# Optimization experiments

Hardware: AMD Instinct MI355X
Metric: run time of the kernel (lower is better)

The kernel has to match this reference:

```python
import jax, jax.numpy as jnp
import numpy as np

COMMITMENT_COST = 0.25
CODEBOOK_SIZE = 1024
EMBED_DIM = 128


def setup_inputs() -> dict:
    key = jax.random.key(0)
    k1, k2 = jax.random.split(key)
    z = jax.random.normal(k1, (16, 2048, EMBED_DIM), dtype=jnp.float32)
    codebook = jax.random.normal(k2, (CODEBOOK_SIZE, EMBED_DIM), dtype=jnp.float32) / (EMBED_DIM ** 0.5)
    return {"z": z, "codebook": codebook}


def reference(z, codebook):
    B, N, D = z.shape
    K = codebook.shape[0]
    flat = z.reshape(-1, D)  # [M, D]

    distances = (
        jnp.sum(flat * flat, axis=1, keepdims=True)
        - 2.0 * flat @ codebook.T
        + jnp.sum(codebook * codebook, axis=1)[None, :]
    )
    indices = jnp.argmin(distances, axis=1)  # [M]

    # one_hot @ codebook == direct gather
    quantized = codebook[indices].reshape(B, N, D)

    codebook_loss = jnp.mean((quantized - z) ** 2)
    commit_loss = COMMITMENT_COST * jnp.mean((z - quantized) ** 2)

    # straight-through (no grad in pure fwd, same values)
    z_q = quantized

    # avg_probs = mean of one-hot encodings = code usage frequency
    M = flat.shape[0]
    counts = jax.ops.segment_sum(jnp.ones((M,), dtype=z.dtype), indices, num_segments=K)
    avg_probs = counts / M
    perplexity = jnp.exp(-jnp.sum(avg_probs * jnp.log(avg_probs + 1e-10)))

    return (
        z_q,
        indices.reshape(B, N),
        commit_loss,
        codebook_loss,
        perplexity,
        distances.reshape(B, N, K),
    )
```

## Files before the change

kernel.cpp:

```cpp
#include <hip/hip_runtime.h>
#include <math.h>

#define D 128
#define K 1024
#define BM 32
#define BN 32
#define NCH (K / BN)
#define CHB 16384

typedef __attribute__((ext_vector_type(8))) short bf16x8;
typedef __attribute__((ext_vector_type(4))) float f32x4;
typedef unsigned short u16;


__device__ __forceinline__ u16 f2bf(float x) {
    union { float f; unsigned u; } v; v.f = x;
    unsigned r = (v.u + 0x7FFFu + ((v.u >> 16) & 1u)) >> 16;
    return (u16)r;
}
__device__ __forceinline__ float bf2f(u16 b) {
    union { float f; unsigned u; } v; v.u = ((unsigned)b) << 16;
    return v.f;
}
__device__ __forceinline__ void gll16(const void* g, void* l) {
    __builtin_amdgcn_global_load_lds(
        (const __attribute__((address_space(1))) void*)g,
        (__attribute__((address_space(3))) void*)l, 16, 0, 0);
}

__global__ void prep_cb(const float* __restrict__ cb, u16* __restrict__ frag,
                        float* __restrict__ cnorm) {
    int tid = blockIdx.x * blockDim.x + threadIdx.x;
    int code = tid >> 5, d4 = tid & 31;
    float4 v = reinterpret_cast<const float4*>(cb)[tid];
    u16 h0 = f2bf(v.x), h1 = f2bf(v.y), h2 = f2bf(v.z), h3 = f2bf(v.w);
    u16 l0 = f2bf(v.x - bf2f(h0)), l1 = f2bf(v.y - bf2f(h1));
    u16 l2 = f2bf(v.z - bf2f(h2)), l3 = f2bf(v.w - bf2f(h3));
    int c = code >> 5, row = code & 31;
    int sb = (row * 256 + d4 * 8) ^ ((row & 7) << 4);
    char* base = (char*)frag + (size_t)c * CHB;
    *reinterpret_cast<ushort4*>(base + sb) = make_ushort4(h0, h1, h2, h3);
    *reinterpret_cast<ushort4*>(base + 8192 + sb) = make_ushort4(l0, l1, l2, l3);
    float s = v.x * v.x + v.y * v.y + v.z * v.z + v.w * v.w;
#pragma unroll
    for (int m = 1; m <= 16; m <<= 1) s += __shfl_xor(s, m);
    if (d4 == 0) cnorm[code] = s;
}

__global__ __launch_bounds__(256, 4)
void vq_main(const float* __restrict__ z, const float* __restrict__ codebook,
             const float* __restrict__ cnorm, const u16* __restrict__ frag,
             int* __restrict__ hist, float* __restrict__ loss_accum,
             float* __restrict__ out_zq, float* __restrict__ out_idx,
             float* __restrict__ out_dist) {
    __shared__ u16 Bsh[2][8192];
    __shared__ float cn_s[K];
    __shared__ float xn_s[BM];
    __shared__ int bi_s[BM], si_s[BM], best_s[BM];

    const int t = threadIdx.x;
    const int lane = t & 63;
    const int wave = t >> 6;
    const int lr = lane & 15, lg = lane >> 4;
    const int rowgrp = wave & 1, colhalf = wave >> 1;
    const int row_base = blockIdx.x * BM;

    if (t < BM) xn_s[t] = 0.f;
#pragma unroll
    for (int k = 0; k < 4; ++k) cn_s[t + k * 256] = cnorm[t + k * 256];
    __syncthreads();

    {
        const float4* zg = reinterpret_cast<const float4*>(z + (size_t)row_base * D);
#pragma unroll
        for (int k = 0; k < 4; ++k) {
            int f = t + k * 256;
            int r = f >> 5, d4 = f & 31;
            float4 v = zg[f];
            u16 h0 = f2bf(v.x), h1 = f2bf(v.y), h2 = f2bf(v.z), h3 = f2bf(v.w);
            u16 l0 = f2bf(v.x - bf2f(h0)), l1 = f2bf(v.y - bf2f(h1));
            u16 l2 = f2bf(v.z - bf2f(h2)), l3 = f2bf(v.w - bf2f(h3));
            int sb = (r * 256 + d4 * 8) ^ ((r & 7) << 4);
            *reinterpret_cast<ushort4*>((char*)Bsh + sb) = make_ushort4(h0, h1, h2, h3);
            *reinterpret_cast<ushort4*>((char*)Bsh + 8192 + sb) = make_ushort4(l0, l1, l2, l3);
            atomicAdd(&xn_s[r], v.x * v.x + v.y * v.y + v.z * v.z + v.w * v.w);
        }
    }
    __syncthreads();

    const int arow = rowgrp * 16 + lr;
    bf16x8 zh[4], zl[4];
#pragma unroll
    for (int kb = 0; kb < 4; ++kb) {
        int sb = (arow * 256 + kb * 64 + lg * 16) ^ ((arow & 7) << 4);
        zh[kb] = *reinterpret_cast<const bf16x8*>((char*)Bsh + sb);
        zl[kb] = *reinterpret_cast<const bf16x8*>((char*)Bsh + 8192 + sb);
    }
    const float xn = xn_s[arow];

    const char* fsrc = (const char*)frag + t * 16;
    {
        char* dst = (char*)Bsh + 16384 + t * 16;
#pragma unroll
        for (int it = 0; it < 4; ++it) gll16(fsrc + it * 4096, dst + it * 4096);
    }
    __syncthreads();

    float v1 = INFINITY, v2 = INFINITY;
    int i1 = K, i2 = K;
    int cur = 1;
    const int myrow = row_base + rowgrp * 16 + lr;
    float* orow = out_dist + (size_t)myrow * K + colhalf * 16 + lg * 4;
    const int crow = colhalf * 16 + lr;

    for (int c = 0; c < NCH; ++c) {
        if (c < NCH - 1) {
            const char* src = fsrc + (size_t)(c + 1) * CHB;
            char* dst = (char*)Bsh + (cur ^ 1) * 16384 + t * 16;
#pragma unroll
            for (int it = 0; it < 4; ++it) gll16(src + it * 4096, dst + it * 4096);
        }

        const char* bb = (const char*)Bsh + cur * 16384;
        f32x4 acc = {0.f, 0.f, 0.f, 0.f};
#pragma unroll
        for (int kb = 0; kb < 4; ++kb) {
            int sb = (crow * 256 + kb * 64 + lg * 16) ^ ((crow & 7) << 4);
            bf16x8 ch = *reinterpret_cast<const bf16x8*>(bb + sb);
            bf16x8 cl = *reinterpret_cast<const bf16x8*>(bb + 8192 + sb);
            acc = __builtin_amdgcn_mfma_f32_16x16x32_bf16(ch, zh[kb], acc, 0, 0, 0);
            acc = __builtin_amdgcn_mfma_f32_16x16x32_bf16(ch, zl[kb], acc, 0, 0, 0);
            acc = __builtin_amdgcn_mfma_f32_16x16x32_bf16(cl, zh[kb], acc, 0, 0, 0);
        }

        const int cbase = c * BN + colhalf * 16 + lg * 4;
        float4 cn4 = *reinterpret_cast<const float4*>(&cn_s[cbase]);
        float d0 = fmaf(-2.f, acc[0], xn + cn4.x);
        float d1 = fmaf(-2.f, acc[1], xn + cn4.y);
        float d2 = fmaf(-2.f, acc[2], xn + cn4.z);
        float d3 = fmaf(-2.f, acc[3], xn + cn4.w);
        if (d0 < v1) { v2 = v1; i2 = i1; v1 = d0; i1 = cbase; }
        else if (d0 < v2) { v2 = d0; i2 = cbase; }
        if (d1 < v1) { v2 = v1; i2 = i1; v1 = d1; i1 = cbase + 1; }
        else if (d1 < v2) { v2 = d1; i2 = cbase + 1; }
        if (d2 < v1) { v2 = v1; i2 = i1; v1 = d2; i1 = cbase + 2; }
        else if (d2 < v2) { v2 = d2; i2 = cbase + 2; }
        if (d3 < v1) { v2 = v1; i2 = i1; v1 = d3; i1 = cbase + 3; }
        else if (d3 < v2) { v2 = d3; i2 = cbase + 3; }
        *reinterpret_cast<float4*>(orow + (size_t)c * BN) = make_float4(d0, d1, d2, d3);

        __syncthreads();
        cur ^= 1;
    }

    float* rv1 = reinterpret_cast<float*>(Bsh);
    float* rv2 = rv1 + 256;
    int* ri1 = reinterpret_cast<int*>(rv2 + 256);
    int* ri2 = ri1 + 256;
    {
        const int slot = colhalf * 4 + lg;
        const int rr = rowgrp * 16 + lr;
        rv1[slot * 32 + rr] = v1;
        rv2[slot * 32 + rr] = v2;
        ri1[slot * 32 + rr] = i1;
        ri2[slot * 32 + rr] = i2;
    }
    __syncthreads();

    if (t < BM) {
        float bv = INFINITY, sv = INFINITY;
        int bi = K, si = K;
        for (int s = 0; s < 8; ++s) {
            float cv1 = rv1[s * 32 + t]; int ci1 = ri1[s * 32 + t];
            float cv2 = rv2[s * 32 + t]; int ci2 = ri2[s * 32 + t];
            if (cv1 < bv || (cv1 == bv && ci1 < bi)) { sv = bv; si = bi; bv = cv1; bi = ci1; }
            else if (cv1 < sv || (cv1 == sv && ci1 < si)) { sv = cv1; si = ci1; }
            if (cv2 < bv || (cv2 == bv && ci2 < bi)) { sv = bv; si = bi; bv = cv2; bi = ci2; }
            else if (cv2 < sv || (cv2 == sv && ci2 < si)) { sv = cv2; si = ci2; }
        }
        bi_s[t] = bi;
        si_s[t] = si;
    }
    __syncthreads();

    float lossv = 0.f;
    if (t < 128) {
        const int rr = t >> 2, t4 = t & 3;
        const int bi = bi_s[rr], si = si_s[rr];
        const float4* zr = reinterpret_cast<const float4*>(z + (size_t)(row_base + rr) * D);
        const float4* c1 = reinterpret_cast<const float4*>(codebook + (size_t)bi * D);
        const float4* c2 = reinterpret_cast<const float4*>(codebook + (size_t)si * D);
        double dd1 = 0.0, dd2 = 0.0;
#pragma unroll
        for (int j = 0; j < 8; ++j) {
            float4 xv = zr[t4 * 8 + j];
            float4 a = c1[t4 * 8 + j];
            float4 b = c2[t4 * 8 + j];
            double e;
            e = (double)xv.x - (double)a.x; dd1 += e * e;
            e = (double)xv.y - (double)a.y; dd1 += e * e;
            e = (double)xv.z - (double)a.z; dd1 += e * e;
            e = (double)xv.w - (double)a.w; dd1 += e * e;
            e = (double)xv.x - (double)b.x; dd2 += e * e;
            e = (double)xv.y - (double)b.y; dd2 += e * e;
            e = (double)xv.z - (double)b.z; dd2 += e * e;
            e = (double)xv.w - (double)b.w; dd2 += e * e;
        }
        dd1 += __shfl_xor(dd1, 1); dd1 += __shfl_xor(dd1, 2);
        dd2 += __shfl_xor(dd2, 1); dd2 += __shfl_xor(dd2, 2);
        if (t4 == 0) {
            int fi = bi; double dmin = dd1;
            if (dd2 < dd1 || (dd2 == dd1 && si < bi)) { fi = si; dmin = dd2; }
            best_s[rr] = fi;
            out_idx[row_base + rr] = (float)fi;
            atomicAdd(&hist[fi], 1);
            lossv = (float)dmin;
        }
    }
#pragma unroll
    for (int o = 32; o > 0; o >>= 1) lossv += __shfl_down(lossv, o);
    if (lane == 0) atomicAdd(loss_accum, lossv);
    __syncthreads();

    {
        const float4* cb4 = reinterpret_cast<const float4*>(codebook);
        float4* zq4 = reinterpret_cast<float4*>(out_zq + (size_t)row_base * D);
#pragma unroll
        for (int k = 0; k < 4; ++k) {
            int f = t + k * 256;
            int r = f >> 5, d4 = f & 31;
            zq4[f] = cb4[(size_t)best_s[r] * 32 + d4];
        }
    }
}

__global__ void vq_finalize(const int* __restrict__ hist, const float* __restrict__ loss_accum,
                            float* __restrict__ out_scalars, int M) {
    __shared__ float red[256];
    int t = threadIdx.x;
    float s = 0.f;
    float invM = 1.0f / (float)M;
#pragma unroll
    for (int k = 0; k < K / 256; ++k) {
        float p = (float)hist[t + k * 256] * invM;
        s += p * logf(p + 1e-10f);
    }
    red[t] = s;
    __syncthreads();
    for (int off = 128; off > 0; off >>= 1) {
        if (t < off) red[t] += red[t + off];
        __syncthreads();
    }
    if (t == 0) {
        float loss = loss_accum[0] / ((float)M * (float)D);
        out_scalars[0] = 0.25f * loss;
        out_scalars[1] = loss;
        out_scalars[2] = expf(-red[0]);
    }
}

extern "C" void kernel_launch(void* const* d_in, const int* in_sizes, int n_in,
                              void* d_out, int out_size, void* d_ws, size_t ws_size,
                              hipStream_t stream) {
    const float* z = (const float*)d_in[0];
    const float* codebook = (const float*)d_in[1];
    int M = in_sizes[0] / D;

    float* out = (float*)d_out;
    float* out_zq = out;
    float* out_idx = out + (size_t)M * D;
    float* out_scalars = out_idx + M;
    float* out_dist = out_scalars + 3;

    int* hist = (int*)d_ws;
    float* loss_accum = (float*)((char*)d_ws + 4096);
    float* cnorm = (float*)((char*)d_ws + 8192);
    u16* frag = (u16*)((char*)d_ws + 16384);

    hipMemsetAsync(d_ws, 0, 8192, stream);
    prep_cb<<<(K * D / 4) / 256, 256, 0, stream>>>(codebook, frag, cnorm);
    vq_main<<<M / BM, 256, 0, stream>>>(z, codebook, cnorm, frag, hist, loss_accum,
                                        out_zq, out_idx, out_dist);
    vq_finalize<<<1, 256, 0, stream>>>(hist, loss_accum, out_scalars, M);
}
```

Before: 114.4 us.

## Hold codebook fragments in registers and split distance and merge kernels

```diff
diff --git a/kernel.cpp b/kernel.cpp
--- a/kernel.cpp
+++ b/kernel.cpp
@@ -3,30 +3,265 @@
 
 #define D 128
 #define K 1024
+
+typedef __attribute__((ext_vector_type(8))) short bf16x8;
+typedef __attribute__((ext_vector_type(4))) float f32x4;
+typedef unsigned short u16;
+
+
+__device__ __forceinline__ u16 f2bf(float x) {
+    union { float f; unsigned u; } v; v.f = x;
+    unsigned r = (v.u + 0x7FFFu + ((v.u >> 16) & 1u)) >> 16;
+    return (u16)r;
+}
+__device__ __forceinline__ float bf2f(u16 b) {
+    union { float f; unsigned u; } v; v.u = ((unsigned)b) << 16;
+    return v.f;
+}
+__device__ __forceinline__ void gll16(const void* g, void* l) {
+    __builtin_amdgcn_global_load_lds(
+        (const __attribute__((address_space(1))) void*)g,
+        (__attribute__((address_space(3))) void*)l, 16, 0, 0);
+}
+
+__device__ __forceinline__ void t2merge(float& v1, int& i1, float& v2, int& i2,
+                                        float bv1, int bi1, float bv2, int bi2) {
+    if (bv1 < v1 || (bv1 == v1 && bi1 < i1)) {
+        v2 = v1; i2 = i1;
+        v1 = bv1; i1 = bi1;
+        if (bv2 < v2 || (bv2 == v2 && bi2 < i2)) { v2 = bv2; i2 = bi2; }
+    } else {
+        if (bv1 < v2 || (bv1 == v2 && bi1 < i2)) { v2 = bv1; i2 = bi1; }
+    }
+}
+
+
+__global__ void prep2(const float* __restrict__ cb, u16* __restrict__ frag,
+                      float* __restrict__ cnorm) {
+    int tid = blockIdx.x * blockDim.x + threadIdx.x;
+    int code = tid >> 5, d4 = tid & 31;
+    float4 v = reinterpret_cast<const float4*>(cb)[tid];
+    u16 h0 = f2bf(v.x), h1 = f2bf(v.y), h2 = f2bf(v.z), h3 = f2bf(v.w);
+    u16 l0 = f2bf(v.x - bf2f(h0)), l1 = f2bf(v.y - bf2f(h1));
+    u16 l2 = f2bf(v.z - bf2f(h2)), l3 = f2bf(v.w - bf2f(h3));
+    u16* base = frag + (size_t)code * 256;
+    *reinterpret_cast<ushort4*>(base + d4 * 4) = make_ushort4(h0, h1, h2, h3);
+    *reinterpret_cast<ushort4*>(base + 128 + d4 * 4) = make_ushort4(l0, l1, l2, l3);
+    float s = v.x * v.x + v.y * v.y + v.z * v.z + v.w * v.w;
+#pragma unroll
+    for (int m = 1; m <= 16; m <<= 1) s += __shfl_xor(s, m);
+    if (d4 == 0) cnorm[code] = s;
+}
+
+__global__ __launch_bounds__(512, 8)
+void vq_dist(const float* __restrict__ z, const u16* __restrict__ frag,
+             const float* __restrict__ cnorm, float4* __restrict__ part,
+             float* __restrict__ out_dist) {
+    __shared__ u16 zsh[16384];
+    __shared__ float cn_s[512];
+    __shared__ float xn_s[64];
+
+    const int t = threadIdx.x;
+    const int lane = t & 63;
+    const int wave = t >> 6;
+    const int lr = lane & 15, lg = lane >> 4;
+    const int rg = blockIdx.x >> 1, cg = blockIdx.x & 1;
+    const int row_base = rg * 64;
+
+    if (t < 64) xn_s[t] = 0.f;
+    if (t < 512) cn_s[t] = cnorm[cg * 512 + t];
+    __syncthreads();
+
+    {
+        const float4* zg = reinterpret_cast<const float4*>(z + (size_t)row_base * D);
+#pragma unroll
+        for (int k = 0; k < 4; ++k) {
+            int f = t + k * 512;
+            int r = f >> 5, d4 = f & 31;
+            float4 v = zg[f];
+            u16 h0 = f2bf(v.x), h1 = f2bf(v.y), h2 = f2bf(v.z), h3 = f2bf(v.w);
+            u16 l0 = f2bf(v.x - bf2f(h0)), l1 = f2bf(v.y - bf2f(h1));
+            u16 l2 = f2bf(v.z - bf2f(h2)), l3 = f2bf(v.w - bf2f(h3));
+            int sb = (r * 256 + d4 * 8) ^ ((r & 7) << 4);
+            *reinterpret_cast<ushort4*>((char*)zsh + sb) = make_ushort4(h0, h1, h2, h3);
+            *reinterpret_cast<ushort4*>((char*)zsh + 16384 + sb) = make_ushort4(l0, l1, l2, l3);
+            atomicAdd(&xn_s[r], v.x * v.x + v.y * v.y + v.z * v.z + v.w * v.w);
+        }
+    }
+
+    bf16x8 ch[4][4], cl[4][4];
+    {
+        const u16* cbase = frag + (size_t)(cg * 512 + wave * 64) * 256;
+#pragma unroll
+        for (int nt = 0; nt < 4; ++nt)
+#pragma unroll
+            for (int kb = 0; kb < 4; ++kb) {
+                const u16* p = cbase + (size_t)(nt * 16 + lr) * 256 + kb * 32 + lg * 8;
+                ch[nt][kb] = *reinterpret_cast<const bf16x8*>(p);
+                cl[nt][kb] = *reinterpret_cast<const bf16x8*>(p + 128);
+            }
+    }
+    __syncthreads();
+
+    float v1[4], v2[4];
+    int i1[4], i2[4];
+#pragma unroll
+    for (int s = 0; s < 4; ++s) { v1[s] = INFINITY; v2[s] = INFINITY; i1[s] = K; i2[s] = K; }
+
+    const int code0 = cg * 512 + wave * 64;
+
+#pragma unroll
+    for (int s = 0; s < 4; ++s) {
+        f32x4 acc[4];
+#pragma unroll
+        for (int nt = 0; nt < 4; ++nt) { acc[nt][0] = 0.f; acc[nt][1] = 0.f; acc[nt][2] = 0.f; acc[nt][3] = 0.f; }
+
+#pragma unroll
+        for (int kb = 0; kb < 4; ++kb) {
+            int zrow = s * 16 + lr;
+            int sb = (zrow * 256 + kb * 64 + lg * 16) ^ ((zrow & 7) << 4);
+            bf16x8 zh = *reinterpret_cast<const bf16x8*>((char*)zsh + sb);
+            bf16x8 zl = *reinterpret_cast<const bf16x8*>((char*)zsh + 16384 + sb);
+#pragma unroll
+            for (int nt = 0; nt < 4; ++nt) {
+                acc[nt] = __builtin_amdgcn_mfma_f32_16x16x32_bf16(ch[nt][kb], zh, acc[nt], 0, 0, 0);
+                acc[nt] = __builtin_amdgcn_mfma_f32_16x16x32_bf16(ch[nt][kb], zl, acc[nt], 0, 0, 0);
+                acc[nt] = __builtin_amdgcn_mfma_f32_16x16x32_bf16(cl[nt][kb], zh, acc[nt], 0, 0, 0);
+            }
+        }
+
+        const int myrow = row_base + s * 16 + lr;
+        const float xn = xn_s[s * 16 + lr];
+        float* orow = out_dist + (size_t)myrow * K + code0 + lg * 4;
+#pragma unroll
+        for (int nt = 0; nt < 4; ++nt) {
+            float4 cn4 = *reinterpret_cast<const float4*>(&cn_s[wave * 64 + nt * 16 + lg * 4]);
+            int cb0 = code0 + nt * 16 + lg * 4;
+            float d0 = fmaf(-2.f, acc[nt][0], xn + cn4.x);
+            float d1 = fmaf(-2.f, acc[nt][1], xn + cn4.y);
+            float d2 = fmaf(-2.f, acc[nt][2], xn + cn4.z);
+            float d3 = fmaf(-2.f, acc[nt][3], xn + cn4.w);
+            if (d0 < v1[s]) { v2[s] = v1[s]; i2[s] = i1[s]; v1[s] = d0; i1[s] = cb0; }
+            else if (d0 < v2[s]) { v2[s] = d0; i2[s] = cb0; }
+            if (d1 < v1[s]) { v2[s] = v1[s]; i2[s] = i1[s]; v1[s] = d1; i1[s] = cb0 + 1; }
+            else if (d1 < v2[s]) { v2[s] = d1; i2[s] = cb0 + 1; }
+            if (d2 < v1[s]) { v2[s] = v1[s]; i2[s] = i1[s]; v1[s] = d2; i1[s] = cb0 + 2; }
+            else if (d2 < v2[s]) { v2[s] = d2; i2[s] = cb0 + 2; }
+            if (d3 < v1[s]) { v2[s] = v1[s]; i2[s] = i1[s]; v1[s] = d3; i1[s] = cb0 + 3; }
+            else if (d3 < v2[s]) { v2[s] = d3; i2[s] = cb0 + 3; }
+            f32x4 dv = {d0, d1, d2, d3};
+            __builtin_nontemporal_store(dv, reinterpret_cast<f32x4*>(orow + nt * 16));
+        }
+    }
+
+#pragma unroll
+    for (int s = 0; s < 4; ++s) {
+#pragma unroll
+        for (int m = 16; m <= 32; m <<= 1) {
+            float bv1 = __shfl_xor(v1[s], m), bv2 = __shfl_xor(v2[s], m);
+            int bi1 = __shfl_xor(i1[s], m), bi2 = __shfl_xor(i2[s], m);
+            t2merge(v1[s], i1[s], v2[s], i2[s], bv1, bi1, bv2, bi2);
+        }
+    }
+
+    __syncthreads();
+    float4* scr = reinterpret_cast<float4*>(zsh);
+    if (lane < 16) {
+#pragma unroll
+        for (int s = 0; s < 4; ++s) {
+            int row = s * 16 + lane;
+            float4 p;
+            p.x = v1[s]; p.y = v2[s];
+            p.z = __int_as_float(i1[s]); p.w = __int_as_float(i2[s]);
+            scr[row * 8 + wave] = p;
+        }
+    }
+    __syncthreads();
+
+    if (t < 64) {
+        float bv = INFINITY, sv = INFINITY;
+        int bi = K, si = K;
+        for (int w = 0; w < 8; ++w) {
+            float4 p = scr[t * 8 + w];
+            t2merge(bv, bi, sv, si, p.x, __float_as_int(p.z), p.y, __float_as_int(p.w));
+        }
+        float4 o;
+        o.x = bv; o.y = sv;
+        o.z = __int_as_float(bi); o.w = __int_as_float(si);
+        part[(size_t)(row_base + t) * 2 + cg] = o;
+    }
+}
+
+__global__ __launch_bounds__(256)
+void vq_merge(const float* __restrict__ z, const float* __restrict__ codebook,
+              const float4* __restrict__ part, int* __restrict__ hist,
+              float* __restrict__ loss_accum, float* __restrict__ out_zq,
+              float* __restrict__ out_idx) {
+    __shared__ int best_s[64];
+    const int t = threadIdx.x;
+    const int lane = t & 63;
+    const int row0 = blockIdx.x * 64;
+    const int rr = t >> 2, t4 = t & 3;
+    const int row = row0 + rr;
+
+    float4 pa = part[(size_t)row * 2];
+    float4 pb = part[(size_t)row * 2 + 1];
+    float v1 = pa.x, v2 = pa.y;
+    int i1 = __float_as_int(pa.z), i2 = __float_as_int(pa.w);
+    t2merge(v1, i1, v2, i2, pb.x, __float_as_int(pb.z), pb.y, __float_as_int(pb.w));
+    const int bi = i1, si = i2;
+
+    const float4* zr = reinterpret_cast<const float4*>(z + (size_t)row * D);
+    const float4* c1 = reinterpret_cast<const float4*>(codebook + (size_t)bi * D);
+    const float4* c2 = reinterpret_cast<const float4*>(codebook + (size_t)si * D);
+    double dd1 = 0.0, dd2 = 0.0;
+#pragma unroll
+    for (int j = 0; j < 8; ++j) {
+        float4 xv = zr[t4 * 8 + j];
+        float4 a = c1[t4 * 8 + j];
+        float4 b = c2[t4 * 8 + j];
+        double e;
+        e = (double)xv.x - (double)a.x; dd1 += e * e;
+        e = (double)xv.y - (double)a.y; dd1 += e * e;
+        e = (double)xv.z - (double)a.z; dd1 += e * e;
+        e = (double)xv.w - (double)a.w; dd1 += e * e;
+        e = (double)xv.x - (double)b.x; dd2 += e * e;
+        e = (double)xv.y - (double)b.y; dd2 += e * e;
+        e = (double)xv.z - (double)b.z; dd2 += e * e;
+        e = (double)xv.w - (double)b.w; dd2 += e * e;
+    }
+    dd1 += __shfl_xor(dd1, 1); dd1 += __shfl_xor(dd1, 2);
+    dd2 += __shfl_xor(dd2, 1); dd2 += __shfl_xor(dd2, 2);
+    float lossv = 0.f;
+    if (t4 == 0) {
+        int fi = bi; double dmin = dd1;
+        if (dd2 < dd1 || (dd2 == dd1 && si < bi)) { fi = si; dmin = dd2; }
+        best_s[rr] = fi;
+        out_idx[row] = (float)fi;
+        atomicAdd(&hist[fi], 1);
+        lossv = (float)dmin;
+    }
+#pragma unroll
+    for (int o = 32; o > 0; o >>= 1) lossv += __shfl_down(lossv, o);
+    if (lane == 0) atomicAdd(loss_accum, lossv);
+    __syncthreads();
+
+    const float4* cb4 = reinterpret_cast<const float4*>(codebook);
+    float4* zq4 = reinterpret_cast<float4*>(out_zq + (size_t)row0 * D);
+#pragma unroll
+    for (int k = 0; k < 8; ++k) {
+        int f = t + k * 256;
+        int r = f >> 5, d4 = f & 31;
+        float4 q = cb4[(size_t)best_s[r] * 32 + d4];
+        f32x4 qv = {q.x, q.y, q.z, q.w};
+        __builtin_nontemporal_store(qv, reinterpret_cast<f32x4*>(&zq4[f]));
+    }
+}
+
 #define BM 32
 #define BN 32
 #define NCH (K / BN)
 #define CHB 16384
-
-typedef __attribute__((ext_vector_type(8))) short bf16x8;
-typedef __attribute__((ext_vector_type(4))) float f32x4;
-typedef unsigned short u16;
-
-
-__device__ __forceinline__ u16 f2bf(float x) {
-    union { float f; unsigned u; } v; v.f = x;
-    unsigned r = (v.u + 0x7FFFu + ((v.u >> 16) & 1u)) >> 16;
-    return (u16)r;
-}
-__device__ __forceinline__ float bf2f(u16 b) {
-    union { float f; unsigned u; } v; v.u = ((unsigned)b) << 16;
-    return v.f;
-}
-__device__ __forceinline__ void gll16(const void* g, void* l) {
-    __builtin_amdgcn_global_load_lds(
-        (const __attribute__((address_space(1))) void*)g,
-        (__attribute__((address_space(3))) void*)l, 16, 0, 0);
-}
 
 __global__ void prep_cb(const float* __restrict__ cb, u16* __restrict__ frag,
                         float* __restrict__ cnorm) {
@@ -126,11 +361,11 @@
 #pragma unroll
         for (int kb = 0; kb < 4; ++kb) {
             int sb = (crow * 256 + kb * 64 + lg * 16) ^ ((crow & 7) << 4);
-            bf16x8 ch = *reinterpret_cast<const bf16x8*>(bb + sb);
-            bf16x8 cl = *reinterpret_cast<const bf16x8*>(bb + 8192 + sb);
-            acc = __builtin_amdgcn_mfma_f32_16x16x32_bf16(ch, zh[kb], acc, 0, 0, 0);
-            acc = __builtin_amdgcn_mfma_f32_16x16x32_bf16(ch, zl[kb], acc, 0, 0, 0);
-            acc = __builtin_amdgcn_mfma_f32_16x16x32_bf16(cl, zh[kb], acc, 0, 0, 0);
+            bf16x8 chh = *reinterpret_cast<const bf16x8*>(bb + sb);
+            bf16x8 cll = *reinterpret_cast<const bf16x8*>(bb + 8192 + sb);
+            acc = __builtin_amdgcn_mfma_f32_16x16x32_bf16(chh, zh[kb], acc, 0, 0, 0);
+            acc = __builtin_amdgcn_mfma_f32_16x16x32_bf16(chh, zl[kb], acc, 0, 0, 0);
+            acc = __builtin_amdgcn_mfma_f32_16x16x32_bf16(cll, zh[kb], acc, 0, 0, 0);
         }
 
         const int cbase = c * BN + colhalf * 16 + lg * 4;
@@ -171,12 +406,7 @@
         float bv = INFINITY, sv = INFINITY;
         int bi = K, si = K;
         for (int s = 0; s < 8; ++s) {
-            float cv1 = rv1[s * 32 + t]; int ci1 = ri1[s * 32 + t];
-            float cv2 = rv2[s * 32 + t]; int ci2 = ri2[s * 32 + t];
-            if (cv1 < bv || (cv1 == bv && ci1 < bi)) { sv = bv; si = bi; bv = cv1; bi = ci1; }
-            else if (cv1 < sv || (cv1 == sv && ci1 < si)) { sv = cv1; si = ci1; }
-            if (cv2 < bv || (cv2 == bv && ci2 < bi)) { sv = bv; si = bi; bv = cv2; bi = ci2; }
-            else if (cv2 < sv || (cv2 == sv && ci2 < si)) { sv = cv2; si = ci2; }
+            t2merge(bv, bi, sv, si, rv1[s * 32 + t], ri1[s * 32 + t], rv2[s * 32 + t], ri2[s * 32 + t]);
         }
         bi_s[t] = bi;
         si_s[t] = si;
@@ -276,10 +506,18 @@
     float* loss_accum = (float*)((char*)d_ws + 4096);
     float* cnorm = (float*)((char*)d_ws + 8192);
     u16* frag = (u16*)((char*)d_ws + 16384);
+    float4* part = (float4*)((char*)d_ws + 540672);
 
     hipMemsetAsync(d_ws, 0, 8192, stream);
-    prep_cb<<<(K * D / 4) / 256, 256, 0, stream>>>(codebook, frag, cnorm);
-    vq_main<<<M / BM, 256, 0, stream>>>(z, codebook, cnorm, frag, hist, loss_accum,
-                                        out_zq, out_idx, out_dist);
+    if (ws_size >= (size_t)540672 + (size_t)M * 32) {
+        prep2<<<(K * D / 4) / 256, 256, 0, stream>>>(codebook, frag, cnorm);
+        vq_dist<<<(M / 64) * 2, 512, 0, stream>>>(z, frag, cnorm, part, out_dist);
+        vq_merge<<<M / 64, 256, 0, stream>>>(z, codebook, part, hist, loss_accum,
+                                             out_zq, out_idx);
+    } else {
+        prep_cb<<<(K * D / 4) / 256, 256, 0, stream>>>(codebook, frag, cnorm);
+        vq_main<<<M / BM, 256, 0, stream>>>(z, codebook, cnorm, frag, hist, loss_accum,
+                                            out_zq, out_idx, out_dist);
+    }
     vq_finalize<<<1, 256, 0, stream>>>(hist, loss_accum, out_scalars, M);
 }
```

After: 445.6 us. 290% more time.

## Keep codebook fragments in registers and stream z rows from LDS

Applied to the files above, without the earlier changes.

```diff
diff --git a/kernel.cpp b/kernel.cpp
--- a/kernel.cpp
+++ b/kernel.cpp
@@ -3,10 +3,6 @@
 
 #define D 128
 #define K 1024
-#define BM 32
-#define BN 32
-#define NCH (K / BN)
-#define CHB 16384
 
 typedef __attribute__((ext_vector_type(8))) short bf16x8;
 typedef __attribute__((ext_vector_type(4))) float f32x4;
@@ -22,161 +18,162 @@
     union { float f; unsigned u; } v; v.u = ((unsigned)b) << 16;
     return v.f;
 }
-__device__ __forceinline__ void gll16(const void* g, void* l) {
-    __builtin_amdgcn_global_load_lds(
-        (const __attribute__((address_space(1))) void*)g,
-        (__attribute__((address_space(3))) void*)l, 16, 0, 0);
-}
-
-__global__ void prep_cb(const float* __restrict__ cb, u16* __restrict__ frag,
-                        float* __restrict__ cnorm) {
+
+__device__ __forceinline__ void t2merge(float& v1, int& i1, float& v2, int& i2,
+                                        float bv1, int bi1, float bv2, int bi2) {
+    if (bv1 < v1 || (bv1 == v1 && bi1 < i1)) {
+        v2 = v1; i2 = i1;
+        v1 = bv1; i1 = bi1;
+        if (bv2 < v2 || (bv2 == v2 && bi2 < i2)) { v2 = bv2; i2 = bi2; }
+    } else {
+        if (bv1 < v2 || (bv1 == v2 && bi1 < i2)) { v2 = bv1; i2 = bi1; }
+    }
+}
+
+__global__ void prep2(const float* __restrict__ cb, u16* __restrict__ frag,
+                      float* __restrict__ cnorm, int* __restrict__ hist,
+                      float* __restrict__ loss_accum) {
     int tid = blockIdx.x * blockDim.x + threadIdx.x;
+    if (tid < K) hist[tid] = 0;
+    if (tid == K) loss_accum[0] = 0.f;
     int code = tid >> 5, d4 = tid & 31;
     float4 v = reinterpret_cast<const float4*>(cb)[tid];
     u16 h0 = f2bf(v.x), h1 = f2bf(v.y), h2 = f2bf(v.z), h3 = f2bf(v.w);
     u16 l0 = f2bf(v.x - bf2f(h0)), l1 = f2bf(v.y - bf2f(h1));
     u16 l2 = f2bf(v.z - bf2f(h2)), l3 = f2bf(v.w - bf2f(h3));
-    int c = code >> 5, row = code & 31;
-    int sb = (row * 256 + d4 * 8) ^ ((row & 7) << 4);
-    char* base = (char*)frag + (size_t)c * CHB;
-    *reinterpret_cast<ushort4*>(base + sb) = make_ushort4(h0, h1, h2, h3);
-    *reinterpret_cast<ushort4*>(base + 8192 + sb) = make_ushort4(l0, l1, l2, l3);
+    u16* base = frag + (size_t)code * 256;
+    *reinterpret_cast<ushort4*>(base + d4 * 4) = make_ushort4(h0, h1, h2, h3);
+    *reinterpret_cast<ushort4*>(base + 128 + d4 * 4) = make_ushort4(l0, l1, l2, l3);
     float s = v.x * v.x + v.y * v.y + v.z * v.z + v.w * v.w;
 #pragma unroll
     for (int m = 1; m <= 16; m <<= 1) s += __shfl_xor(s, m);
     if (d4 == 0) cnorm[code] = s;
 }
 
-__global__ __launch_bounds__(256, 4)
-void vq_main(const float* __restrict__ z, const float* __restrict__ codebook,
-             const float* __restrict__ cnorm, const u16* __restrict__ frag,
-             int* __restrict__ hist, float* __restrict__ loss_accum,
-             float* __restrict__ out_zq, float* __restrict__ out_idx,
-             float* __restrict__ out_dist) {
-    __shared__ u16 Bsh[2][8192];
+__global__ __launch_bounds__(512, 2)
+void vq_all(const float* __restrict__ z, const float* __restrict__ codebook,
+            const u16* __restrict__ frag, const float* __restrict__ cnorm,
+            int* __restrict__ hist, float* __restrict__ loss_accum,
+            float* __restrict__ out_zq, float* __restrict__ out_idx,
+            float* __restrict__ out_dist) {
+    __shared__ u16 zsh[16384];
+    __shared__ float4 scr[16 * 64];
     __shared__ float cn_s[K];
-    __shared__ float xn_s[BM];
-    __shared__ int bi_s[BM], si_s[BM], best_s[BM];
+    __shared__ float xn_s[64];
+    __shared__ int bi_s[64], si_s[64], best_s[64];
 
     const int t = threadIdx.x;
     const int lane = t & 63;
     const int wave = t >> 6;
     const int lr = lane & 15, lg = lane >> 4;
-    const int rowgrp = wave & 1, colhalf = wave >> 1;
-    const int row_base = blockIdx.x * BM;
-
-    if (t < BM) xn_s[t] = 0.f;
-#pragma unroll
-    for (int k = 0; k < 4; ++k) cn_s[t + k * 256] = cnorm[t + k * 256];
+    const int row_base = blockIdx.x * 64;
+
+    if (t < 64) xn_s[t] = 0.f;
+    cn_s[t] = cnorm[t];
+    cn_s[t + 512] = cnorm[t + 512];
     __syncthreads();
 
     {
         const float4* zg = reinterpret_cast<const float4*>(z + (size_t)row_base * D);
 #pragma unroll
         for (int k = 0; k < 4; ++k) {
-            int f = t + k * 256;
+            int f = t + k * 512;
             int r = f >> 5, d4 = f & 31;
             float4 v = zg[f];
             u16 h0 = f2bf(v.x), h1 = f2bf(v.y), h2 = f2bf(v.z), h3 = f2bf(v.w);
             u16 l0 = f2bf(v.x - bf2f(h0)), l1 = f2bf(v.y - bf2f(h1));
             u16 l2 = f2bf(v.z - bf2f(h2)), l3 = f2bf(v.w - bf2f(h3));
             int sb = (r * 256 + d4 * 8) ^ ((r & 7) << 4);
-            *reinterpret_cast<ushort4*>((char*)Bsh + sb) = make_ushort4(h0, h1, h2, h3);
-            *reinterpret_cast<ushort4*>((char*)Bsh + 8192 + sb) = make_ushort4(l0, l1, l2, l3);
+            *reinterpret_cast<ushort4*>((char*)zsh + sb) = make_ushort4(h0, h1, h2, h3);
+            *reinterpret_cast<ushort4*>((char*)zsh + 16384 + sb) = make_ushort4(l0, l1, l2, l3);
             atomicAdd(&xn_s[r], v.x * v.x + v.y * v.y + v.z * v.z + v.w * v.w);
         }
     }
     __syncthreads();
 
-    const int arow = rowgrp * 16 + lr;
-    bf16x8 zh[4], zl[4];
-#pragma unroll
-    for (int kb = 0; kb < 4; ++kb) {
-        int sb = (arow * 256 + kb * 64 + lg * 16) ^ ((arow & 7) << 4);
-        zh[kb] = *reinterpret_cast<const bf16x8*>((char*)Bsh + sb);
-        zl[kb] = *reinterpret_cast<const bf16x8*>((char*)Bsh + 8192 + sb);
-    }
-    const float xn = xn_s[arow];
-
-    const char* fsrc = (const char*)frag + t * 16;
-    {
-        char* dst = (char*)Bsh + 16384 + t * 16;
-#pragma unroll
-        for (int it = 0; it < 4; ++it) gll16(fsrc + it * 4096, dst + it * 4096);
-    }
-    __syncthreads();
-
-    float v1 = INFINITY, v2 = INFINITY;
-    int i1 = K, i2 = K;
-    int cur = 1;
-    const int myrow = row_base + rowgrp * 16 + lr;
-    float* orow = out_dist + (size_t)myrow * K + colhalf * 16 + lg * 4;
-    const int crow = colhalf * 16 + lr;
-
-    for (int c = 0; c < NCH; ++c) {
-        if (c < NCH - 1) {
-            const char* src = fsrc + (size_t)(c + 1) * CHB;
-            char* dst = (char*)Bsh + (cur ^ 1) * 16384 + t * 16;
-#pragma unroll
-            for (int it = 0; it < 4; ++it) gll16(src + it * 4096, dst + it * 4096);
-        }
-
-        const char* bb = (const char*)Bsh + cur * 16384;
-        f32x4 acc = {0.f, 0.f, 0.f, 0.f};
-#pragma unroll
-        for (int kb = 0; kb < 4; ++kb) {
-            int sb = (crow * 256 + kb * 64 + lg * 16) ^ ((crow & 7) << 4);
-            bf16x8 ch = *reinterpret_cast<const bf16x8*>(bb + sb);
-            bf16x8 cl = *reinterpret_cast<const bf16x8*>(bb + 8192 + sb);
-            acc = __builtin_amdgcn_mfma_f32_16x16x32_bf16(ch, zh[kb], acc, 0, 0, 0);
-            acc = __builtin_amdgcn_mfma_f32_16x16x32_bf16(ch, zl[kb], acc, 0, 0, 0);
-            acc = __builtin_amdgcn_mfma_f32_16x16x32_bf16(cl, zh[kb], acc, 0, 0, 0);
-        }
-
-        const int cbase = c * BN + colhalf * 16 + lg * 4;
-        float4 cn4 = *reinterpret_cast<const float4*>(&cn_s[cbase]);
-        float d0 = fmaf(-2.f, acc[0], xn + cn4.x);
-        float d1 = fmaf(-2.f, acc[1], xn + cn4.y);
-        float d2 = fmaf(-2.f, acc[2], xn + cn4.z);
-        float d3 = fmaf(-2.f, acc[3], xn + cn4.w);
-        if (d0 < v1) { v2 = v1; i2 = i1; v1 = d0; i1 = cbase; }
-        else if (d0 < v2) { v2 = d0; i2 = cbase; }
-        if (d1 < v1) { v2 = v1; i2 = i1; v1 = d1; i1 = cbase + 1; }
-        else if (d1 < v2) { v2 = d1; i2 = cbase + 1; }
-        if (d2 < v1) { v2 = v1; i2 = i1; v1 = d2; i1 = cbase + 2; }
-        else if (d2 < v2) { v2 = d2; i2 = cbase + 2; }
-        if (d3 < v1) { v2 = v1; i2 = i1; v1 = d3; i1 = cbase + 3; }
-        else if (d3 < v2) { v2 = d3; i2 = cbase + 3; }
-        *reinterpret_cast<float4*>(orow + (size_t)c * BN) = make_float4(d0, d1, d2, d3);
-
-        __syncthreads();
-        cur ^= 1;
-    }
-
-    float* rv1 = reinterpret_cast<float*>(Bsh);
-    float* rv2 = rv1 + 256;
-    int* ri1 = reinterpret_cast<int*>(rv2 + 256);
-    int* ri2 = ri1 + 256;
-    {
-        const int slot = colhalf * 4 + lg;
-        const int rr = rowgrp * 16 + lr;
-        rv1[slot * 32 + rr] = v1;
-        rv2[slot * 32 + rr] = v2;
-        ri1[slot * 32 + rr] = i1;
-        ri2[slot * 32 + rr] = i2;
-    }
-    __syncthreads();
-
-    if (t < BM) {
+#pragma unroll 1
+    for (int cg = 0; cg < 2; ++cg) {
+        bf16x8 ch[4][4], cl[4][4];
+        {
+            const u16* cbase = frag + (size_t)(cg * 512 + wave * 64) * 256;
+#pragma unroll
+            for (int nt = 0; nt < 4; ++nt)
+#pragma unroll
+                for (int kb = 0; kb < 4; ++kb) {
+                    const u16* p = cbase + (size_t)(nt * 16 + lr) * 256 + kb * 32 + lg * 8;
+                    ch[nt][kb] = *reinterpret_cast<const bf16x8*>(p);
+                    cl[nt][kb] = *reinterpret_cast<const bf16x8*>(p + 128);
+                }
+        }
+        const int code0 = cg * 512 + wave * 64;
+
+#pragma unroll 1
+        for (int s = 0; s < 4; ++s) {
+            f32x4 acc[4];
+#pragma unroll
+            for (int nt = 0; nt < 4; ++nt) { acc[nt][0] = 0.f; acc[nt][1] = 0.f; acc[nt][2] = 0.f; acc[nt][3] = 0.f; }
+
+            const int zrow = s * 16 + lr;
+#pragma unroll
+            for (int kb = 0; kb < 4; ++kb) {
+                int sb = (zrow * 256 + kb * 64 + lg * 16) ^ ((zrow & 7) << 4);
+                bf16x8 zh = *reinterpret_cast<const bf16x8*>((char*)zsh + sb);
+                bf16x8 zl = *reinterpret_cast<const bf16x8*>((char*)zsh + 16384 + sb);
+#pragma unroll
+                for (int nt = 0; nt < 4; ++nt) {
+                    acc[nt] = __builtin_amdgcn_mfma_f32_16x16x32_bf16(ch[nt][kb], zh, acc[nt], 0, 0, 0);
+                    acc[nt] = __builtin_amdgcn_mfma_f32_16x16x32_bf16(ch[nt][kb], zl, acc[nt], 0, 0, 0);
+                    acc[nt] = __builtin_amdgcn_mfma_f32_16x16x32_bf16(cl[nt][kb], zh, acc[nt], 0, 0, 0);
+                }
+            }
+
+            const float xn = xn_s[zrow];
+            float* orow = out_dist + (size_t)(row_base + zrow) * K + code0 + lg * 4;
+            float v1 = INFINITY, v2 = INFINITY;
+            int i1 = K, i2 = K;
+#pragma unroll
+            for (int nt = 0; nt < 4; ++nt) {
+                float4 cn4 = *reinterpret_cast<const float4*>(&cn_s[code0 + nt * 16 + lg * 4]);
+                int cb0 = code0 + nt * 16 + lg * 4;
+                float d0 = fmaf(-2.f, acc[nt][0], xn + cn4.x);
+                float d1 = fmaf(-2.f, acc[nt][1], xn + cn4.y);
+                float d2 = fmaf(-2.f, acc[nt][2], xn + cn4.z);
+                float d3 = fmaf(-2.f, acc[nt][3], xn + cn4.w);
+                if (d0 < v1) { v2 = v1; i2 = i1; v1 = d0; i1 = cb0; }
+                else if (d0 < v2) { v2 = d0; i2 = cb0; }
+                if (d1 < v1) { v2 = v1; i2 = i1; v1 = d1; i1 = cb0 + 1; }
+                else if (d1 < v2) { v2 = d1; i2 = cb0 + 1; }
+                if (d2 < v1) { v2 = v1; i2 = i1; v1 = d2; i1 = cb0 + 2; }
+                else if (d2 < v2) { v2 = d2; i2 = cb0 + 2; }
+                if (d3 < v1) { v2 = v1; i2 = i1; v1 = d3; i1 = cb0 + 3; }
+                else if (d3 < v2) { v2 = d3; i2 = cb0 + 3; }
+                f32x4 dv = {d0, d1, d2, d3};
+                *reinterpret_cast<f32x4*>(orow + nt * 16) = dv;
+            }
+
+#pragma unroll
+            for (int m = 16; m <= 32; m <<= 1) {
+                float bv1 = __shfl_xor(v1, m), bv2 = __shfl_xor(v2, m);
+                int bi1 = __shfl_xor(i1, m), bi2 = __shfl_xor(i2, m);
+                t2merge(v1, i1, v2, i2, bv1, bi1, bv2, bi2);
+            }
+            if (lane < 16) {
+                float4 p;
+                p.x = v1; p.y = v2;
+                p.z = __int_as_float(i1); p.w = __int_as_float(i2);
+                scr[(cg * 8 + wave) * 64 + (s * 16 + lane)] = p;
+            }
+        }
+    }
+    __syncthreads();
+
+    if (t < 64) {
         float bv = INFINITY, sv = INFINITY;
         int bi = K, si = K;
-        for (int s = 0; s < 8; ++s) {
-            float cv1 = rv1[s * 32 + t]; int ci1 = ri1[s * 32 + t];
-            float cv2 = rv2[s * 32 + t]; int ci2 = ri2[s * 32 + t];
-            if (cv1 < bv || (cv1 == bv && ci1 < bi)) { sv = bv; si = bi; bv = cv1; bi = ci1; }
-            else if (cv1 < sv || (cv1 == sv && ci1 < si)) { sv = cv1; si = ci1; }
-            if (cv2 < bv || (cv2 == bv && ci2 < bi)) { sv = bv; si = bi; bv = cv2; bi = ci2; }
-            else if (cv2 < sv || (cv2 == sv && ci2 < si)) { sv = cv2; si = ci2; }
+#pragma unroll
+        for (int j = 0; j < 16; ++j) {
+            float4 p = scr[j * 64 + t];
+            t2merge(bv, bi, sv, si, p.x, __float_as_int(p.z), p.y, __float_as_int(p.w));
         }
         bi_s[t] = bi;
         si_s[t] = si;
@@ -184,7 +181,7 @@
     __syncthreads();
 
     float lossv = 0.f;
-    if (t < 128) {
+    if (t < 256) {
         const int rr = t >> 2, t4 = t & 3;
         const int bi = bi_s[rr], si = si_s[rr];
         const float4* zr = reinterpret_cast<const float4*>(z + (size_t)(row_base + rr) * D);
@@ -227,7 +224,7 @@
         float4* zq4 = reinterpret_cast<float4*>(out_zq + (size_t)row_base * D);
 #pragma unroll
         for (int k = 0; k < 4; ++k) {
-            int f = t + k * 256;
+            int f = t + k * 512;
             int r = f >> 5, d4 = f & 31;
             zq4[f] = cb4[(size_t)best_s[r] * 32 + d4];
         }
@@ -277,9 +274,8 @@
     float* cnorm = (float*)((char*)d_ws + 8192);
     u16* frag = (u16*)((char*)d_ws + 16384);
 
-    hipMemsetAsync(d_ws, 0, 8192, stream);
-    prep_cb<<<(K * D / 4) / 256, 256, 0, stream>>>(codebook, frag, cnorm);
-    vq_main<<<M / BM, 256, 0, stream>>>(z, codebook, cnorm, frag, hist, loss_accum,
-                                        out_zq, out_idx, out_dist);
+    prep2<<<(K * D / 4) / 256, 256, 0, stream>>>(codebook, frag, cnorm, hist, loss_accum);
+    vq_all<<<M / 64, 512, 0, stream>>>(z, codebook, frag, cnorm, hist, loss_accum,
+                                       out_zq, out_idx, out_dist);
     vq_finalize<<<1, 256, 0, stream>>>(hist, loss_accum, out_scalars, M);
 }
```

Result: slower. 130.9 us (+14.4%).
